# Performance work log

Hardware: AMD Instinct MI355X
Metric: run time of the kernel (lower is better)

## Reference

```python
import jax, jax.numpy as jnp
import numpy as np

N_NODES = 2000
LN_EPS = 1e-5
NEG_SLOPE = 0.2  # PyG GATConv default


def _gat(xg, W, b, a_src, a_dst, src, dst):
    # xg: [G, N, Fin]; single-head GATConv, add_self_loops=False
    h = xg @ W                      # [G, N, H]
    es = h @ a_src                  # [G, N]
    ed = h @ a_dst                  # [G, N]
    e = jax.nn.leaky_relu(es[:, src] + ed[:, dst], NEG_SLOPE)  # [G, E]

    def seg_softmax(e_g):
        m = jax.ops.segment_max(e_g, dst, num_segments=N_NODES)
        ex = jnp.exp(e_g - m[dst])
        s = jax.ops.segment_sum(ex, dst, num_segments=N_NODES)
        return ex / (s[dst] + 1e-16)

    alpha = jax.vmap(seg_softmax)(e)            # [G, E]
    msg = alpha[..., None] * h[:, src]          # [G, E, H]
    agg = jax.vmap(lambda m_: jax.ops.segment_sum(m_, dst, num_segments=N_NODES))(msg)
    return agg + b                              # [G, N, H]


def _gcn_layer(x, W, b, a_src, a_dst, src, dst):
    # x: [B, N, T, F] -- faithfully replicate original permute + raw reshape
    B, N, T, F = x.shape
    x_in = jnp.transpose(x, (0, 2, 1, 3)).reshape(B * T, N, F)
    out = _gat(x_in, W, b, a_src, a_dst, src, dst)          # [B*T, N, H]
    out = jax.nn.gelu(out.reshape(B, T, N, -1), approximate=False)
    # original does .reshape(B, N, T, -1) on a [B,T,N,H]-contiguous tensor
    return out.reshape(B, N, T, -1)


def _lstm(x, Wih, Whh, bih, bhh):
    # x: [BN, T, Fin]; torch LSTM gate order i,f,g,o
    BN, T, _ = x.shape
    H = Whh.shape[1]
    xz = x @ Wih.T + (bih + bhh)                # [BN, T, 4H]

    def step(carry, z_t):
        h, c = carry
        z = z_t + h @ Whh.T
        i, f, g, o = jnp.split(z, 4, axis=-1)
        c = jax.nn.sigmoid(f) * c + jax.nn.sigmoid(i) * jnp.tanh(g)
        h = jax.nn.sigmoid(o) * jnp.tanh(c)
        return (h, c), h

    init = (jnp.zeros((BN, H), x.dtype), jnp.zeros((BN, H), x.dtype))
    _, hs = jax.lax.scan(step, init, jnp.swapaxes(xz, 0, 1))
    return jnp.swapaxes(hs, 0, 1)               # [BN, T, H]


def setup_inputs() -> dict:
    key = jax.random.key(0)
    ks = jax.random.split(key, 20)
    B, N, T, NX, H, PL, NY, E = 2, N_NODES, 24, 8, 64, 12, 1, 32000
    p = {}
    p["x"] = jax.random.normal(ks[0], (B, N, T, NX), jnp.float32)
    p["edge_src"] = jax.random.randint(ks[1], (E,), 0, N, jnp.int32)
    p["edge_dst"] = jax.random.randint(ks[2], (E,), 0, N, jnp.int32)
    p["fc_W"] = jax.random.normal(ks[3], (NX, H), jnp.float32) / np.sqrt(NX)
    p["fc_b"] = jnp.zeros((H,), jnp.float32)
    for i, tag in enumerate(["g1", "g2"]):
        p[f"{tag}_W"] = jax.random.normal(ks[4 + 4 * i], (H, H), jnp.float32) / np.sqrt(H)
        p[f"{tag}_b"] = jnp.zeros((H,), jnp.float32)
        p[f"{tag}_asrc"] = jax.random.normal(ks[5 + 4 * i], (H,), jnp.float32) / np.sqrt(H)
        p[f"{tag}_adst"] = jax.random.normal(ks[6 + 4 * i], (H,), jnp.float32) / np.sqrt(H)
    p["lstm_Wih"] = jax.random.normal(ks[12], (4 * H, H), jnp.float32) / np.sqrt(H)
    p["lstm_Whh"] = jax.random.normal(ks[13], (4 * H, H), jnp.float32) / np.sqrt(H)
    p["lstm_bih"] = jnp.zeros((4 * H,), jnp.float32)
    p["lstm_bhh"] = jnp.zeros((4 * H,), jnp.float32)
    p["ln_g"] = jnp.ones((H,), jnp.float32)
    p["ln_b"] = jnp.zeros((H,), jnp.float32)
    p["dense_W"] = jax.random.normal(ks[14], (H, PL * NY), jnp.float32) / np.sqrt(H)
    p["dense_b"] = jnp.zeros((PL * NY,), jnp.float32)
    return p


def reference(x, edge_src, edge_dst, fc_W, fc_b,
              g1_W, g1_b, g1_asrc, g1_adst,
              g2_W, g2_b, g2_asrc, g2_adst,
              lstm_Wih, lstm_Whh, lstm_bih, lstm_bhh,
              ln_g, ln_b, dense_W, dense_b):
    B, N, T, _ = x.shape
    PRED_LEN, NY = 12, 1
    x_h = x @ fc_W + fc_b                                        # [B,N,T,H]
    g1 = _gcn_layer(x_h, g1_W, g1_b, g1_asrc, g1_adst, edge_src, edge_dst)
    g2 = _gcn_layer(g1, g2_W, g2_b, g2_asrc, g2_adst, edge_src, edge_dst)
    H = g2.shape[-1]
    lout = _lstm(g2.reshape(B * N, T, -1), lstm_Wih, lstm_Whh, lstm_bih, lstm_bhh)
    lout = lout.reshape(B, N, T, H)
    mu = jnp.mean(lout, axis=-1, keepdims=True)
    var = jnp.mean(jnp.square(lout - mu), axis=-1, keepdims=True)
    h = (lout - mu) / jnp.sqrt(var + LN_EPS) * ln_g + ln_b
    out = h[:, :, -1:, :] @ dense_W + dense_b                    # [B,N,1,PL*NY]
    return out.reshape(B, N, PRED_LEN, NY)
```

## Files before the change

### kernel.cpp

```cpp
#include <hip/hip_runtime.h>
#include <hip/hip_bf16.h>
#include <math.h>

#define B_   2
#define N_   2000
#define T_   24
#define NX_  8
#define H_   64
#define G_   (B_*T_)
#define E_   32000
#define BN_  (B_*N_)
#define TH_  (T_*H_)
#define NTH_ (N_*T_*H_)
#define GNH_ (G_*N_*H_)
#define NPARAM_ 43340
#define NPARAM_PAD_ 43392
#define LSTM_PAD 72

using bf16 = __hip_bfloat16;
typedef short bf16x8 __attribute__((ext_vector_type(8)));
typedef float f32x4  __attribute__((ext_vector_type(4)));

__device__ __forceinline__ float uasf(unsigned u){ return __uint_as_float(u); }
__device__ __forceinline__ float wave_sum(float v){
  #pragma unroll
  for (int o = 32; o > 0; o >>= 1) v += __shfl_xor(v, o, 64);
  return v;
}
__device__ __forceinline__ float half_sum(float v){
  #pragma unroll
  for (int o = 16; o > 0; o >>= 1) v += __shfl_xor(v, o, 64);
  return v;
}
__device__ __forceinline__ float half_max(float v){
  #pragma unroll
  for (int o = 16; o > 0; o >>= 1) v = fmaxf(v, __shfl_xor(v, o, 64));
  return v;
}
__device__ __forceinline__ float fastrcp(float x){ return __builtin_amdgcn_rcpf(x); }
__device__ __forceinline__ float sigf(float x){ return fastrcp(1.f + __expf(-x)); }
__device__ __forceinline__ float tanhfast(float x){ return 1.f - 2.f*fastrcp(1.f + __expf(2.f*x)); }
__device__ __forceinline__ float gelu_exact(float x){ return 0.5f*x*(1.f + erff(x*0.70710678118654752f)); }
__device__ __forceinline__ unsigned f2bf_rtn(float f){
  unsigned u = __float_as_uint(f);
  u += 0x7fffu + ((u >> 16) & 1u);
  return u >> 16;
}
__device__ __forceinline__ bf16x8 pack8(float4 a, float4 b){
  bf16x8 v;
  v[0]=(short)f2bf_rtn(a.x); v[1]=(short)f2bf_rtn(a.y);
  v[2]=(short)f2bf_rtn(a.z); v[3]=(short)f2bf_rtn(a.w);
  v[4]=(short)f2bf_rtn(b.x); v[5]=(short)f2bf_rtn(b.y);
  v[6]=(short)f2bf_rtn(b.z); v[7]=(short)f2bf_rtn(b.w);
  return v;
}

__global__ void detect_kernel(const unsigned* __restrict__ xw, int* __restrict__ flag){
  __shared__ int cnt;
  if (threadIdx.x == 0) cnt = 0;
  __syncthreads();
  int c = 0;
  for (int i = threadIdx.x; i < 4096; i += 256){
    unsigned e = (xw[i] >> 7) & 0xffu;
    if (e >= 100u && e <= 140u) c++;
  }
  atomicAdd(&cnt, c);
  __syncthreads();
  if (threadIdx.x == 0) *flag = (cnt > 3276) ? 1 : 0;
}

struct ConvArgs {
  const void* src[18];
  int off[19];
};
__global__ __launch_bounds__(256) void convert_kernel(
    ConvArgs a, const int* __restrict__ flag, float* __restrict__ dst){
  int i = blockIdx.x*256 + threadIdx.x;
  if (i >= NPARAM_) return;
  int seg = 0;
  while (i >= a.off[seg+1]) seg++;
  int j = i - a.off[seg];
  float v;
  if (*flag){
    v = uasf(((unsigned)((const unsigned short*)a.src[seg])[j]) << 16);
  } else {
    v = ((const float*)a.src[seg])[j];
  }
  dst[i] = v;
}

__global__ void wc_kernel(const float* __restrict__ fcW, const float* __restrict__ fcb,
                          const float* __restrict__ g1W,
                          float* __restrict__ wc, float* __restrict__ bc){
  int tid = threadIdx.x;
  int i = tid >> 6, n = tid & 63;
  float s = 0.f;
  #pragma unroll 8
  for (int k = 0; k < 64; ++k) s = fmaf(fcW[i*64 + k], g1W[k*64 + n], s);
  wc[i*64 + n] = s;
  if (i == 0){
    float b = 0.f;
    #pragma unroll 8
    for (int k = 0; k < 64; ++k) b = fmaf(fcb[k], g1W[k*64 + n], b);
    bc[n] = b;
  }
}

__global__ void zero_kernel(int* p, int n){
  int i = blockIdx.x*256 + threadIdx.x;
  if (i < n) p[i] = 0;
}
__global__ void count_kernel(const int* __restrict__ dst, int* __restrict__ counts){
  int e = blockIdx.x*256 + threadIdx.x;
  if (e < E_) atomicAdd(&counts[dst[e]], 1);
}
__global__ void scan_kernel(const int* __restrict__ counts, int* __restrict__ offs){
  int lane = threadIdx.x & 63;
  int base = 0;
  for (int c0 = 0; c0 < N_; c0 += 64){
    int i = c0 + lane;
    int v = (i < N_) ? counts[i] : 0;
    int xv = v;
    #pragma unroll
    for (int o = 1; o < 64; o <<= 1){
      int y = __shfl_up(xv, o, 64);
      if (lane >= o) xv += y;
    }
    if (i < N_) offs[i] = base + xv - v;
    base += __shfl(xv, 63, 64);
  }
  if (lane == 0) offs[N_] = base;
}
__global__ void fill_kernel(const int* __restrict__ src, const int* __restrict__ dst,
                            const int* __restrict__ offs, int* __restrict__ cursor,
                            int* __restrict__ csrc){
  int e = blockIdx.x*256 + threadIdx.x;
  if (e >= E_) return;
  int d = dst[e];
  int pos = atomicAdd(&cursor[d], 1);
  csrc[offs[d] + pos] = src[e];
}

__global__ __launch_bounds__(256) void gat_h1_fused_kernel(
    const void* __restrict__ xraw, const int* __restrict__ flag,
    const float* __restrict__ wc, const float* __restrict__ bc,
    const float* __restrict__ asrc, const float* __restrict__ adst,
    unsigned short* __restrict__ hbuf, float* __restrict__ es, float* __restrict__ ed){
  int lane = threadIdx.x & 63, wave = threadIdx.x >> 6;
  int q = lane >> 4, c = lane & 15;
  int isbf = *flag;
  bf16x8 Bf[4];
  #pragma unroll
  for (int nt = 0; nt < 4; ++nt){
    bf16x8 v;
    #pragma unroll
    for (int j = 0; j < 8; ++j)
      v[j] = (q == 0) ? (short)f2bf_rtn(wc[j*64 + nt*16 + c]) : (short)0;
    Bf[nt] = v;
  }
  float bcv[4];
  #pragma unroll
  for (int nt = 0; nt < 4; ++nt) bcv[nt] = bc[nt*16 + c];
  float aS[4], aD[4];
  #pragma unroll
  for (int nt = 0; nt < 4; ++nt){ aS[nt] = asrc[nt*16+c]; aD[nt] = adst[nt*16+c]; }

  int w = blockIdx.x*4 + wave;
  #pragma unroll
  for (int it = 0; it < 2; ++it){
    int tile = w*2 + it;
    int p0 = tile*16;
    int g  = p0 / N_, n0 = p0 - g*N_;
    int bb = g / T_,  tt = g - bb*T_;
    bf16x8 A0;
    #pragma unroll
    for (int j = 0; j < 8; ++j) A0[j] = 0;
    if (q == 0){
      size_t rowelt = ((size_t)(bb*N_ + n0 + c)*T_ + tt)*NX_;
      if (isbf){
        A0 = *(const bf16x8*)((const unsigned short*)xraw + rowelt);
      } else {
        const float4* xr4 = (const float4*)((const float*)xraw + rowelt);
        A0 = pack8(xr4[0], xr4[1]);
      }
    }
    f32x4 acc[4];
    #pragma unroll
    for (int nt = 0; nt < 4; ++nt){ acc[nt][0]=bcv[nt]; acc[nt][1]=bcv[nt]; acc[nt][2]=bcv[nt]; acc[nt][3]=bcv[nt]; }
    #pragma unroll
    for (int nt = 0; nt < 4; ++nt) acc[nt] = __builtin_amdgcn_mfma_f32_16x16x32_bf16(A0, Bf[nt], acc[nt], 0, 0, 0);

    #pragma unroll
    for (int nt = 0; nt < 4; ++nt){
      #pragma unroll
      for (int r = 0; r < 4; ++r)
        hbuf[(size_t)(p0 + q*4 + r)*H_ + nt*16 + c] = (unsigned short)f2bf_rtn(acc[nt][r]);
    }
    #pragma unroll
    for (int r = 0; r < 4; ++r){
      float e1 = acc[0][r]*aS[0] + acc[1][r]*aS[1] + acc[2][r]*aS[2] + acc[3][r]*aS[3];
      float e2 = acc[0][r]*aD[0] + acc[1][r]*aD[1] + acc[2][r]*aD[2] + acc[3][r]*aD[3];
      #pragma unroll
      for (int o = 8; o > 0; o >>= 1){
        e1 += __shfl_xor(e1, o, 64);
        e2 += __shfl_xor(e2, o, 64);
      }
      if (c == 0){
        es[p0 + q*4 + r] = e1;
        ed[p0 + q*4 + r] = e2;
      }
    }
  }
}

__global__ __launch_bounds__(256) void gat_h2_mfma_kernel(
    const float* __restrict__ xin, const float* __restrict__ W,
    const float* __restrict__ asrc, const float* __restrict__ adst,
    unsigned short* __restrict__ hbuf, float* __restrict__ es, float* __restrict__ ed){
  int lane = threadIdx.x & 63, wave = threadIdx.x >> 6;
  int q = lane >> 4, c = lane & 15;
  bf16x8 Bf[4][2];
  #pragma unroll
  for (int nt = 0; nt < 4; ++nt){
    #pragma unroll
    for (int ks = 0; ks < 2; ++ks){
      bf16x8 v;
      #pragma unroll
      for (int j = 0; j < 8; ++j)
        v[j] = (short)f2bf_rtn(W[(ks*32 + q*8 + j)*H_ + nt*16 + c]);
      Bf[nt][ks] = v;
    }
  }
  float aS[4], aD[4];
  #pragma unroll
  for (int nt = 0; nt < 4; ++nt){ aS[nt] = asrc[nt*16+c]; aD[nt] = adst[nt*16+c]; }

  int w = blockIdx.x*4 + wave;
  #pragma unroll
  for (int it = 0; it < 2; ++it){
    int tile = w*2 + it;
    int p0 = tile*16;
    int p  = p0 + c;
    int g = p / N_, n = p - g*N_;
    int bb = g / T_, t = g - bb*T_;
    const float4* xr4 = (const float4*)(xin + (size_t)bb*NTH_ + (size_t)n*TH_ + (size_t)t*H_);
    float4 x0 = xr4[q*2],     x1 = xr4[q*2 + 1];
    float4 x2 = xr4[8 + q*2], x3 = xr4[8 + q*2 + 1];
    bf16x8 A0 = pack8(x0, x1);
    bf16x8 A1 = pack8(x2, x3);

    f32x4 acc[4];
    #pragma unroll
    for (int nt = 0; nt < 4; ++nt){ acc[nt][0]=0.f; acc[nt][1]=0.f; acc[nt][2]=0.f; acc[nt][3]=0.f; }
    #pragma unroll
    for (int nt = 0; nt < 4; ++nt) acc[nt] = __builtin_amdgcn_mfma_f32_16x16x32_bf16(A0, Bf[nt][0], acc[nt], 0, 0, 0);
    #pragma unroll
    for (int nt = 0; nt < 4; ++nt) acc[nt] = __builtin_amdgcn_mfma_f32_16x16x32_bf16(A1, Bf[nt][1], acc[nt], 0, 0, 0);

    #pragma unroll
    for (int nt = 0; nt < 4; ++nt){
      #pragma unroll
      for (int r = 0; r < 4; ++r)
        hbuf[(size_t)(p0 + q*4 + r)*H_ + nt*16 + c] = (unsigned short)f2bf_rtn(acc[nt][r]);
    }
    #pragma unroll
    for (int r = 0; r < 4; ++r){
      float e1 = acc[0][r]*aS[0] + acc[1][r]*aS[1] + acc[2][r]*aS[2] + acc[3][r]*aS[3];
      float e2 = acc[0][r]*aD[0] + acc[1][r]*aD[1] + acc[2][r]*aD[2] + acc[3][r]*aD[3];
      #pragma unroll
      for (int o = 8; o > 0; o >>= 1){
        e1 += __shfl_xor(e1, o, 64);
        e2 += __shfl_xor(e2, o, 64);
      }
      if (c == 0){
        es[p0 + q*4 + r] = e1;
        ed[p0 + q*4 + r] = e2;
      }
    }
  }
}

__global__ __launch_bounds__(256) void gat_agg_kernel(
    const unsigned short* __restrict__ hbuf, const float* __restrict__ es, const float* __restrict__ ed,
    const int* __restrict__ offs, const int* __restrict__ csrc,
    const float* __restrict__ bias, float* __restrict__ gout){
  int lane = threadIdx.x & 63, wave = threadIdx.x >> 6;
  int h = lane >> 5, ln = lane & 31;
  int gd = (blockIdx.x*4 + wave)*2 + h;
  int g = gd / N_, d = gd - g*N_;
  int start = offs[d], deg = offs[d+1] - start;
  const float* esg = es + (size_t)g*N_;
  float edv = ed[(size_t)g*N_ + d];
  const char* hg = (const char*)(hbuf + (size_t)g*N_*H_);
  unsigned lanoff = ((unsigned)ln) << 2;
  int hbase = h << 5;
  int dm = max(deg, __shfl_xor(deg, 32, 64));

  float acc0 = 0.f, acc1 = 0.f;
  if (dm <= 32){
    int sv = 0; float sc = -1e30f;
    if (ln < deg){
      sv = csrc[start + ln];
      float e = esg[sv] + edv;
      sc = e > 0.f ? e : 0.2f*e;
    }
    float m = half_max(sc);
    float ex = (ln < deg) ? __expf(sc - m) : 0.f;
    float ssum = half_sum(ex);
    ex *= fastrcp(ssum + 1e-16f);
    unsigned pw = (f2bf_rtn(ex) << 16) | (unsigned)sv;
    for (int j0 = 0; j0 < dm; j0 += 8){
      unsigned wv[8]; float aa[8]; unsigned off[8];
      #pragma unroll
      for (int u = 0; u < 8; ++u){
        int j = j0 + u;
        wv[u] = (unsigned)__shfl((int)pw, hbase + j, 64);
        aa[u] = (j < deg) ? uasf(wv[u] & 0xffff0000u) : 0.f;
        off[u] = ((wv[u] & 0xffffu) << 7) + lanoff;
      }
      unsigned hv[8];
      #pragma unroll
      for (int u = 0; u < 8; ++u)
        hv[u] = *(const unsigned*)(hg + off[u]);
      #pragma unroll
      for (int u = 0; u < 8; ++u){
        acc0 = fmaf(aa[u], uasf(hv[u] << 16), acc0);
        acc1 = fmaf(aa[u], uasf(hv[u] & 0xffff0000u), acc1);
      }
    }
  } else {
    float m = -1e30f;
    for (int base = 0; base < deg; base += 32){
      int i = base + ln;
      if (i < deg){
        int s = csrc[start + i];
        float e = esg[s] + edv;
        float t = e > 0.f ? e : 0.2f*e;
        m = fmaxf(m, t);
      }
    }
    m = half_max(m);
    float ssum = 0.f;
    for (int base = 0; base < deg; base += 32){
      int i = base + ln;
      if (i < deg){
        int s = csrc[start + i];
        float e = esg[s] + edv;
        float t = e > 0.f ? e : 0.2f*e;
        ssum += __expf(t - m);
      }
    }
    ssum = half_sum(ssum);
    float inv = fastrcp(ssum + 1e-16f);
    for (int base = 0; base < dm; base += 32){
      int i = base + ln;
      int sv = 0; float ex = 0.f;
      if (i < deg){
        sv = csrc[start + i];
        float e = esg[sv] + edv;
        float t = e > 0.f ? e : 0.2f*e;
        ex = __expf(t - m) * inv;
      }
      unsigned pw = (f2bf_rtn(ex) << 16) | (unsigned)sv;
      int rem = dm - base; if (rem > 32) rem = 32;
      int myrem = deg - base;
      for (int j0 = 0; j0 < rem; j0 += 8){
        unsigned wv[8]; float aa[8]; unsigned off[8];
        #pragma unroll
        for (int u = 0; u < 8; ++u){
          int j = j0 + u;
          wv[u] = (unsigned)__shfl((int)pw, hbase + j, 64);
          aa[u] = (j < myrem) ? uasf(wv[u] & 0xffff0000u) : 0.f;
          off[u] = ((wv[u] & 0xffffu) << 7) + lanoff;
        }
        unsigned hv[8];
        #pragma unroll
        for (int u = 0; u < 8; ++u)
          hv[u] = *(const unsigned*)(hg + off[u]);
        #pragma unroll
        for (int u = 0; u < 8; ++u){
          acc0 = fmaf(aa[u], uasf(hv[u] << 16), acc0);
          acc1 = fmaf(aa[u], uasf(hv[u] & 0xffff0000u), acc1);
        }
      }
    }
  }
  float2 bv = ((const float2*)bias)[ln];
  float2 o2;
  o2.x = gelu_exact(acc0 + bv.x);
  o2.y = gelu_exact(acc1 + bv.y);
  ((float2*)(gout + (size_t)gd*H_))[ln] = o2;
}

__global__ __launch_bounds__(256) void lstm_mfma_kernel(
    const float* __restrict__ xin,
    const float* __restrict__ Wih,
    const float* __restrict__ Whh,
    const float* __restrict__ bih, const float* __restrict__ bhh,
    float* __restrict__ hfin){
  __shared__ __align__(16) unsigned short Hlds[16*LSTM_PAD];
  int tid = threadIdx.x;
  int lane = tid & 63, wave = tid >> 6;
  int q = lane >> 4, c = lane & 15;
  int s0 = blockIdx.x * 16;

  bf16x8 Bf[4][4];
  #pragma unroll
  for (int g = 0; g < 4; ++g){
    int n = g*64 + wave*16 + c;
    #pragma unroll
    for (int ks = 0; ks < 4; ++ks){
      const float* srcp = (ks < 2) ? (Whh + (size_t)n*64 + ks*32 + q*8)
                                   : (Wih + (size_t)n*64 + (ks-2)*32 + q*8);
      float4 a = ((const float4*)srcp)[0];
      float4 b = ((const float4*)srcp)[1];
      Bf[g][ks] = pack8(a, b);
    }
  }
  float bsum[4];
  #pragma unroll
  for (int g = 0; g < 4; ++g){
    int n = g*64 + wave*16 + c;
    bsum[g] = bih[n] + bhh[n];
  }
  for (int i = tid; i < 16*LSTM_PAD; i += 256) Hlds[i] = 0;
  float cst[4] = {0.f, 0.f, 0.f, 0.f};
  __syncthreads();

  for (int t = 0; t < T_; ++t){
    const float4* xr4 = (const float4*)(xin + ((size_t)(s0 + c)*T_ + t)*64);
    float4 x0 = xr4[q*2],     x1 = xr4[q*2 + 1];
    float4 x2 = xr4[8 + q*2], x3 = xr4[8 + q*2 + 1];
    bf16x8 Ax0 = pack8(x0, x1);
    bf16x8 Ax1 = pack8(x2, x3);
    const bf16x8* hrow = (const bf16x8*)(Hlds + c*LSTM_PAD);
    bf16x8 Ah0 = hrow[q];
    bf16x8 Ah1 = hrow[4 + q];

    f32x4 acc[4];
    #pragma unroll
    for (int g = 0; g < 4; ++g){ acc[g][0]=bsum[g]; acc[g][1]=bsum[g]; acc[g][2]=bsum[g]; acc[g][3]=bsum[g]; }
    #pragma unroll
    for (int g = 0; g < 4; ++g) acc[g] = __builtin_amdgcn_mfma_f32_16x16x32_bf16(Ah0, Bf[g][0], acc[g], 0, 0, 0);
    #pragma unroll
    for (int g = 0; g < 4; ++g) acc[g] = __builtin_amdgcn_mfma_f32_16x16x32_bf16(Ah1, Bf[g][1], acc[g], 0, 0, 0);
    #pragma unroll
    for (int g = 0; g < 4; ++g) acc[g] = __builtin_amdgcn_mfma_f32_16x16x32_bf16(Ax0, Bf[g][2], acc[g], 0, 0, 0);
    #pragma unroll
    for (int g = 0; g < 4; ++g) acc[g] = __builtin_amdgcn_mfma_f32_16x16x32_bf16(Ax1, Bf[g][3], acc[g], 0, 0, 0);

    float hv[4];
    #pragma unroll
    for (int r = 0; r < 4; ++r){
      float zi = acc[0][r], zf = acc[1][r], zg = acc[2][r], zo = acc[3][r];
      cst[r] = sigf(zf)*cst[r] + sigf(zi)*tanhfast(zg);
      hv[r] = sigf(zo)*tanhfast(cst[r]);
    }
    if (t == T_-1){
      #pragma unroll
      for (int r = 0; r < 4; ++r)
        hfin[(size_t)(s0 + q*4 + r)*64 + wave*16 + c] = hv[r];
    } else {
      __syncthreads();
      #pragma unroll
      for (int r = 0; r < 4; ++r)
        Hlds[(q*4 + r)*LSTM_PAD + wave*16 + c] = (unsigned short)f2bf_rtn(hv[r]);
      __syncthreads();
    }
  }
}

__global__ __launch_bounds__(256) void final_kernel(
    const float* __restrict__ hfin, const float* __restrict__ lng, const float* __restrict__ lnb,
    const float* __restrict__ dW, const float* __restrict__ db,
    const int* __restrict__ flag, void* __restrict__ outv){
  __shared__ float sm[4][64];
  int lane = threadIdx.x & 63, wave = threadIdx.x >> 6;
  int s = blockIdx.x*4 + wave;
  float h = hfin[(size_t)s*64 + lane];
  float mu = wave_sum(h) * (1.f/64.f);
  float dev = h - mu;
  float var = wave_sum(dev*dev) * (1.f/64.f);
  float hn = dev * rsqrtf(var + 1e-5f) * lng[lane] + lnb[lane];
  sm[wave][lane] = hn;
  __syncthreads();
  if (lane < 12){
    float o = db[lane];
    #pragma unroll
    for (int k = 0; k < 64; ++k) o = fmaf(sm[wave][k], dW[k*12 + lane], o);
    if (*flag) ((unsigned short*)outv)[(size_t)s*12 + lane] = (unsigned short)f2bf_rtn(o);
    else       ((float*)outv)[(size_t)s*12 + lane] = o;
  }
}

extern "C" void kernel_launch(void* const* d_in, const int* in_sizes, int n_in,
                              void* d_out, int out_size, void* d_ws, size_t ws_size,
                              hipStream_t stream) {
  const int* esrc = (const int*)d_in[1];
  const int* edst = (const int*)d_in[2];

  static const int sizes[18] = {512, 64, 4096, 64, 64, 64, 4096, 64, 64, 64,
                                16384, 16384, 256, 256, 64, 64, 768, 12};
  static const int srcidx[18] = {3, 4, 5, 6, 7, 8, 9, 10, 11, 12,
                                 13, 14, 15, 16, 17, 18, 19, 20};
  ConvArgs ca;
  {
    int acc = 0;
    for (int i = 0; i < 18; ++i){ ca.src[i] = d_in[srcidx[i]]; ca.off[i] = acc; acc += sizes[i]; }
    ca.off[18] = acc;
  }

  float* P     = (float*)d_ws;
  float* bufA  = P + NPARAM_PAD_;
  float* bufB  = bufA + (size_t)GNH_;
  float* esb   = bufB + (size_t)GNH_;
  float* edb   = esb  + (size_t)G_*N_;
  int*   counts= (int*)(edb + (size_t)G_*N_);
  int*   cursor= counts + N_;
  int*   offs  = cursor + N_;
  int*   csrc  = offs + (N_ + 1);
  int*   flag  = csrc + E_;
  float* wcb   = (float*)(flag + 1);
  unsigned short* hbuf = (unsigned short*)bufB;
  float* hfin  = bufB;

  const float* pfcW = P + 0;
  const float* pfcb = P + 512;
  const float* pg1W = P + 576;
  const float* pg1b = P + 4672;
  const float* pg1as= P + 4736;
  const float* pg1ad= P + 4800;
  const float* pg2W = P + 4864;
  const float* pg2b = P + 8960;
  const float* pg2as= P + 9024;
  const float* pg2ad= P + 9088;
  const float* pWih = P + 9152;
  const float* pWhh = P + 25536;
  const float* pbih = P + 41920;
  const float* pbhh = P + 42176;
  const float* plng = P + 42432;
  const float* plnb = P + 42496;
  const float* pdW  = P + 42560;
  const float* pdb  = P + 43328;

  detect_kernel<<<1, 256, 0, stream>>>((const unsigned*)d_in[0], flag);
  convert_kernel<<<(NPARAM_ + 255)/256, 256, 0, stream>>>(ca, flag, P);
  wc_kernel<<<1, 512, 0, stream>>>(pfcW, pfcb, pg1W, wcb, wcb + 512);

  zero_kernel<<<16, 256, 0, stream>>>(counts, 2*N_);
  count_kernel<<<(E_+255)/256, 256, 0, stream>>>(edst, counts);
  scan_kernel<<<1, 64, 0, stream>>>(counts, offs);
  fill_kernel<<<(E_+255)/256, 256, 0, stream>>>(esrc, edst, offs, cursor, csrc);

  gat_h1_fused_kernel<<<750, 256, 0, stream>>>(d_in[0], flag, wcb, wcb + 512, pg1as, pg1ad, hbuf, esb, edb);
  gat_agg_kernel<<<12000, 256, 0, stream>>>(hbuf, esb, edb, offs, csrc, pg1b, bufA);

  gat_h2_mfma_kernel<<<750, 256, 0, stream>>>(bufA, pg2W, pg2as, pg2ad, hbuf, esb, edb);
  gat_agg_kernel<<<12000, 256, 0, stream>>>(hbuf, esb, edb, offs, csrc, pg2b, bufA);

  lstm_mfma_kernel<<<250, 256, 0, stream>>>(bufA, pWih, pWhh, pbih, pbhh, hfin);
  final_kernel<<<1000, 256, 0, stream>>>(hfin, plng, plnb, pdW, pdb, flag, d_out);
}
```

Before: 266.6 us.

## Merge setup kernels into one prep kernel and fuse LayerNorm/dense into LSTM

Seven small setup launches (dtype detection, parameter conversion, fused weight product, CSR count/scan/fill) are folded into one multi-role prep kernel. Each block re-runs the dtype detection, one block builds the CSR in shared memory, and another computes the fc×g1 weight product straight from the raw inputs. The final LayerNorm and dense projection move into the LSTM kernel's epilogue using shared memory, which removes a global round trip and one launch. The cost is serial CSR construction in a single block and redundant detection reads in every block.

```diff
diff --git a/kernel.cpp b/kernel.cpp
--- a/kernel.cpp
+++ b/kernel.cpp
@@ -55,90 +55,104 @@
   return v;
 }
 
-__global__ void detect_kernel(const unsigned* __restrict__ xw, int* __restrict__ flag){
-  __shared__ int cnt;
-  if (threadIdx.x == 0) cnt = 0;
-  __syncthreads();
-  int c = 0;
-  for (int i = threadIdx.x; i < 4096; i += 256){
-    unsigned e = (xw[i] >> 7) & 0xffu;
-    if (e >= 100u && e <= 140u) c++;
-  }
-  atomicAdd(&cnt, c);
-  __syncthreads();
-  if (threadIdx.x == 0) *flag = (cnt > 3276) ? 1 : 0;
-}
-
 struct ConvArgs {
   const void* src[18];
   int off[19];
 };
-__global__ __launch_bounds__(256) void convert_kernel(
-    ConvArgs a, const int* __restrict__ flag, float* __restrict__ dst){
-  int i = blockIdx.x*256 + threadIdx.x;
-  if (i >= NPARAM_) return;
-  int seg = 0;
-  while (i >= a.off[seg+1]) seg++;
-  int j = i - a.off[seg];
-  float v;
-  if (*flag){
-    v = uasf(((unsigned)((const unsigned short*)a.src[seg])[j]) << 16);
+__global__ __launch_bounds__(256) void prep_kernel(
+    ConvArgs a, const unsigned* __restrict__ xw,
+    const int* __restrict__ esrc, const int* __restrict__ edst,
+    float* __restrict__ dst, int* __restrict__ flag,
+    int* __restrict__ offs, int* __restrict__ csrc,
+    float* __restrict__ wc, float* __restrict__ bc){
+  __shared__ int lcnt[N_];
+  __shared__ int loffs[N_];
+  __shared__ int cnt;
+  int tid = threadIdx.x;
+  if (tid == 0) cnt = 0;
+  __syncthreads();
+  int c = 0;
+  for (int i = tid; i < 4096; i += 256){
+    unsigned e = (xw[i] >> 7) & 0xffu;
+    if (e >= 100u && e <= 140u) c++;
+  }
+  atomicAdd(&cnt, c);
+  __syncthreads();
+  int isbf = (cnt > 3276) ? 1 : 0;
+  int bid = blockIdx.x;
+
+  if (bid < 170){
+    if (bid == 0 && tid == 0) *flag = isbf;
+    int i = bid*256 + tid;
+    if (i < NPARAM_){
+      int seg = 0;
+      while (i >= a.off[seg+1]) seg++;
+      int j = i - a.off[seg];
+      float v;
+      if (isbf) v = uasf(((unsigned)((const unsigned short*)a.src[seg])[j]) << 16);
+      else      v = ((const float*)a.src[seg])[j];
+      dst[i] = v;
+    }
+  } else if (bid == 170){
+    for (int i = tid; i < N_; i += 256) lcnt[i] = 0;
+    __syncthreads();
+    for (int e = tid; e < E_; e += 256) atomicAdd(&lcnt[edst[e]], 1);
+    __syncthreads();
+    if (tid < 64){
+      int lane = tid;
+      int base = 0;
+      for (int c0 = 0; c0 < N_; c0 += 64){
+        int i = c0 + lane;
+        int v = (i < N_) ? lcnt[i] : 0;
+        int xv = v;
+        #pragma unroll
+        for (int o = 1; o < 64; o <<= 1){
+          int y = __shfl_up(xv, o, 64);
+          if (lane >= o) xv += y;
+        }
+        if (i < N_){ int ex = base + xv - v; loffs[i] = ex; offs[i] = ex; }
+        base += __shfl(xv, 63, 64);
+      }
+      if (lane == 0) offs[N_] = base;
+    }
+    __syncthreads();
+    for (int i = tid; i < N_; i += 256) lcnt[i] = 0;
+    __syncthreads();
+    for (int e = tid; e < E_; e += 256){
+      int d = edst[e];
+      int pos = atomicAdd(&lcnt[d], 1);
+      csrc[loffs[d] + pos] = esrc[e];
+    }
   } else {
-    v = ((const float*)a.src[seg])[j];
-  }
-  dst[i] = v;
-}
-
-__global__ void wc_kernel(const float* __restrict__ fcW, const float* __restrict__ fcb,
-                          const float* __restrict__ g1W,
-                          float* __restrict__ wc, float* __restrict__ bc){
-  int tid = threadIdx.x;
-  int i = tid >> 6, n = tid & 63;
-  float s = 0.f;
-  #pragma unroll 8
-  for (int k = 0; k < 64; ++k) s = fmaf(fcW[i*64 + k], g1W[k*64 + n], s);
-  wc[i*64 + n] = s;
-  if (i == 0){
-    float b = 0.f;
-    #pragma unroll 8
-    for (int k = 0; k < 64; ++k) b = fmaf(fcb[k], g1W[k*64 + n], b);
-    bc[n] = b;
-  }
-}
-
-__global__ void zero_kernel(int* p, int n){
-  int i = blockIdx.x*256 + threadIdx.x;
-  if (i < n) p[i] = 0;
-}
-__global__ void count_kernel(const int* __restrict__ dst, int* __restrict__ counts){
-  int e = blockIdx.x*256 + threadIdx.x;
-  if (e < E_) atomicAdd(&counts[dst[e]], 1);
-}
-__global__ void scan_kernel(const int* __restrict__ counts, int* __restrict__ offs){
-  int lane = threadIdx.x & 63;
-  int base = 0;
-  for (int c0 = 0; c0 < N_; c0 += 64){
-    int i = c0 + lane;
-    int v = (i < N_) ? counts[i] : 0;
-    int xv = v;
-    #pragma unroll
-    for (int o = 1; o < 64; o <<= 1){
-      int y = __shfl_up(xv, o, 64);
-      if (lane >= o) xv += y;
-    }
-    if (i < N_) offs[i] = base + xv - v;
-    base += __shfl(xv, 63, 64);
-  }
-  if (lane == 0) offs[N_] = base;
-}
-__global__ void fill_kernel(const int* __restrict__ src, const int* __restrict__ dst,
-                            const int* __restrict__ offs, int* __restrict__ cursor,
-                            int* __restrict__ csrc){
-  int e = blockIdx.x*256 + threadIdx.x;
-  if (e >= E_) return;
-  int d = dst[e];
-  int pos = atomicAdd(&cursor[d], 1);
-  csrc[offs[d] + pos] = src[e];
+    const void* pfcW = a.src[0];
+    const void* pfcb = a.src[1];
+    const void* pg1W = a.src[2];
+    #pragma unroll
+    for (int half = 0; half < 2; ++half){
+      int t2 = half*256 + tid;
+      int i = t2 >> 6, n = t2 & 63;
+      float s = 0.f;
+      for (int k = 0; k < 64; ++k){
+        float fa = isbf ? uasf(((unsigned)((const unsigned short*)pfcW)[i*64+k]) << 16)
+                        : ((const float*)pfcW)[i*64+k];
+        float fb = isbf ? uasf(((unsigned)((const unsigned short*)pg1W)[k*64+n]) << 16)
+                        : ((const float*)pg1W)[k*64+n];
+        s = fmaf(fa, fb, s);
+      }
+      wc[i*64 + n] = s;
+    }
+    if (tid < 64){
+      float b = 0.f;
+      for (int k = 0; k < 64; ++k){
+        float fa = isbf ? uasf(((unsigned)((const unsigned short*)pfcb)[k]) << 16)
+                        : ((const float*)pfcb)[k];
+        float fb = isbf ? uasf(((unsigned)((const unsigned short*)pg1W)[k*64+tid]) << 16)
+                        : ((const float*)pg1W)[k*64+tid];
+        b = fmaf(fa, fb, b);
+      }
+      bc[tid] = b;
+    }
+  }
 }
 
 __global__ __launch_bounds__(256) void gat_h1_fused_kernel(
@@ -392,13 +406,16 @@
   ((float2*)(gout + (size_t)gd*H_))[ln] = o2;
 }
 
-__global__ __launch_bounds__(256) void lstm_mfma_kernel(
+__global__ __launch_bounds__(256) void lstm_final_kernel(
     const float* __restrict__ xin,
     const float* __restrict__ Wih,
     const float* __restrict__ Whh,
     const float* __restrict__ bih, const float* __restrict__ bhh,
-    float* __restrict__ hfin){
+    const float* __restrict__ lng, const float* __restrict__ lnb,
+    const float* __restrict__ dW, const float* __restrict__ db,
+    const int* __restrict__ flag, void* __restrict__ outv){
   __shared__ __align__(16) unsigned short Hlds[16*LSTM_PAD];
+  __shared__ float smH[16][68];
   int tid = threadIdx.x;
   int lane = tid & 63, wave = tid >> 6;
   int q = lane >> 4, c = lane & 15;
@@ -459,7 +476,7 @@
     if (t == T_-1){
       #pragma unroll
       for (int r = 0; r < 4; ++r)
-        hfin[(size_t)(s0 + q*4 + r)*64 + wave*16 + c] = hv[r];
+        smH[q*4 + r][wave*16 + c] = hv[r];
     } else {
       __syncthreads();
       #pragma unroll
@@ -468,28 +485,26 @@
       __syncthreads();
     }
   }
-}
-
-__global__ __launch_bounds__(256) void final_kernel(
-    const float* __restrict__ hfin, const float* __restrict__ lng, const float* __restrict__ lnb,
-    const float* __restrict__ dW, const float* __restrict__ db,
-    const int* __restrict__ flag, void* __restrict__ outv){
-  __shared__ float sm[4][64];
-  int lane = threadIdx.x & 63, wave = threadIdx.x >> 6;
-  int s = blockIdx.x*4 + wave;
-  float h = hfin[(size_t)s*64 + lane];
-  float mu = wave_sum(h) * (1.f/64.f);
-  float dev = h - mu;
-  float var = wave_sum(dev*dev) * (1.f/64.f);
-  float hn = dev * rsqrtf(var + 1e-5f) * lng[lane] + lnb[lane];
-  sm[wave][lane] = hn;
   __syncthreads();
-  if (lane < 12){
-    float o = db[lane];
-    #pragma unroll
-    for (int k = 0; k < 64; ++k) o = fmaf(sm[wave][k], dW[k*12 + lane], o);
-    if (*flag) ((unsigned short*)outv)[(size_t)s*12 + lane] = (unsigned short)f2bf_rtn(o);
-    else       ((float*)outv)[(size_t)s*12 + lane] = o;
+
+  int isbf = *flag;
+  #pragma unroll
+  for (int si = 0; si < 4; ++si){
+    int s = wave*4 + si;
+    float h = smH[s][lane];
+    float mu = wave_sum(h) * (1.f/64.f);
+    float dev = h - mu;
+    float var = wave_sum(dev*dev) * (1.f/64.f);
+    float hn = dev * rsqrtf(var + 1e-5f) * lng[lane] + lnb[lane];
+    smH[s][lane] = hn;
+    if (lane < 12){
+      float o = db[lane];
+      #pragma unroll
+      for (int k = 0; k < 64; ++k) o = fmaf(smH[s][k], dW[k*12 + lane], o);
+      size_t oi = (size_t)(s0 + s)*12 + lane;
+      if (isbf) ((unsigned short*)outv)[oi] = (unsigned short)f2bf_rtn(o);
+      else      ((float*)outv)[oi] = o;
+    }
   }
 }
 
@@ -515,18 +530,12 @@
   float* bufB  = bufA + (size_t)GNH_;
   float* esb   = bufB + (size_t)GNH_;
   float* edb   = esb  + (size_t)G_*N_;
-  int*   counts= (int*)(edb + (size_t)G_*N_);
-  int*   cursor= counts + N_;
-  int*   offs  = cursor + N_;
+  int*   offs  = (int*)(edb + (size_t)G_*N_);
   int*   csrc  = offs + (N_ + 1);
   int*   flag  = csrc + E_;
   float* wcb   = (float*)(flag + 1);
   unsigned short* hbuf = (unsigned short*)bufB;
-  float* hfin  = bufB;
-
-  const float* pfcW = P + 0;
-  const float* pfcb = P + 512;
-  const float* pg1W = P + 576;
+
   const float* pg1b = P + 4672;
   const float* pg1as= P + 4736;
   const float* pg1ad= P + 4800;
@@ -543,21 +552,16 @@
   const float* pdW  = P + 42560;
   const float* pdb  = P + 43328;
 
-  detect_kernel<<<1, 256, 0, stream>>>((const unsigned*)d_in[0], flag);
-  convert_kernel<<<(NPARAM_ + 255)/256, 256, 0, stream>>>(ca, flag, P);
-  wc_kernel<<<1, 512, 0, stream>>>(pfcW, pfcb, pg1W, wcb, wcb + 512);
-
-  zero_kernel<<<16, 256, 0, stream>>>(counts, 2*N_);
-  count_kernel<<<(E_+255)/256, 256, 0, stream>>>(edst, counts);
-  scan_kernel<<<1, 64, 0, stream>>>(counts, offs);
-  fill_kernel<<<(E_+255)/256, 256, 0, stream>>>(esrc, edst, offs, cursor, csrc);
-
-  gat_h1_fused_kernel<<<750, 256, 0, stream>>>(d_in[0], flag, wcb, wcb + 512, pg1as, pg1ad, hbuf, esb, edb);
+  prep_kernel<<<172, 256, 0, stream>>>(ca, (const unsigned*)d_in[0], esrc, edst,
+                                       P, flag, offs, csrc, wcb, wcb + 512);
+
+  gat_h1_fused_kernel<<<750, 256, 0, stream>>>(d_in[0], flag, wcb, wcb + 512,
+                                               pg1as, pg1ad, hbuf, esb, edb);
   gat_agg_kernel<<<12000, 256, 0, stream>>>(hbuf, esb, edb, offs, csrc, pg1b, bufA);
 
   gat_h2_mfma_kernel<<<750, 256, 0, stream>>>(bufA, pg2W, pg2as, pg2ad, hbuf, esb, edb);
   gat_agg_kernel<<<12000, 256, 0, stream>>>(hbuf, esb, edb, offs, csrc, pg2b, bufA);
 
-  lstm_mfma_kernel<<<250, 256, 0, stream>>>(bufA, pWih, pWhh, pbih, pbhh, hfin);
-  final_kernel<<<1000, 256, 0, stream>>>(hfin, plng, plnb, pdW, pdb, flag, d_out);
-}
+  lstm_final_kernel<<<250, 256, 0, stream>>>(bufA, pWih, pWhh, pbih, pbhh,
+                                             plng, plnb, pdW, pdb, flag, d_out);
+}
```

New measurement: 322.8 us. 21.1% more time.
